# Kernel tuning notes

Hardware: AMD Instinct MI355X
Metric: run time of the kernel (lower is better)

Reference implementation:

```python
import jax, jax.numpy as jnp
import numpy as np

B, NELEC, NATOMS, SH_PER_ATOM, NORB, NCTR = 512, 100, 20, 30, 300, 2
NBAS = NATOMS * SH_PER_ATOM  # 600 == NORB * NCTR


def _ipow(x, k):
    # x**k for integer k in {0,1,2}; safe for negative x (cartesian harmonics)
    return jnp.where(k == 0, jnp.ones_like(x), jnp.where(k == 1, x, x * x))


def setup_inputs() -> dict:
    key = jax.random.key(0)
    ks = jax.random.split(key, 7)
    pos = jax.random.normal(ks[0], (B, NELEC * 3), jnp.float32)
    atom_coords = jax.random.normal(ks[1], (NATOMS, 3), jnp.float32)
    bas_exp = jax.random.uniform(ks[2], (NBAS,), jnp.float32, 0.5, 3.0)
    bas_n = jax.random.randint(ks[3], (NBAS,), 0, 3).astype(jnp.float32)
    norm_cst = jax.random.uniform(ks[4], (NBAS,), jnp.float32, 0.5, 1.5)
    bas_coeffs = jax.random.normal(ks[5], (NBAS,), jnp.float32)
    bas_kxyz = jax.random.randint(ks[6], (NBAS, 3), 0, 3)  # kx, ky, kz exponents
    index_ctr = jnp.repeat(jnp.arange(NORB, dtype=jnp.int32), NCTR)  # nbas -> norb
    return {"pos": pos, "atom_coords": atom_coords, "bas_exp": bas_exp,
            "bas_n": bas_n, "norm_cst": norm_cst, "bas_coeffs": bas_coeffs,
            "bas_kxyz": bas_kxyz, "index_ctr": index_ctr}


def reference(pos, atom_coords, bas_exp, bas_n, norm_cst, bas_coeffs, bas_kxyz, index_ctr):
    # gather: per-shell atom coordinates  (NBAS, 3)
    bas_coords = jnp.repeat(atom_coords, SH_PER_ATOM, axis=0)
    # electron - basis-center displacement  (B, Nelec, NBAS, 3)
    xyz = pos.reshape(-1, NELEC, 1, 3) - bas_coords[None, None]
    r2 = jnp.sum(xyz * xyz, axis=-1)                 # (B, Nelec, NBAS)
    r = jnp.sqrt(r2)
    # radial_gaussian: r^n * exp(-alpha r^2)
    R = jnp.power(r, bas_n) * jnp.exp(-bas_exp * r2)
    # cartesian harmonics: x^kx * y^ky * z^kz
    Y = (_ipow(xyz[..., 0], bas_kxyz[:, 0]) *
         _ipow(xyz[..., 1], bas_kxyz[:, 1]) *
         _ipow(xyz[..., 2], bas_kxyz[:, 2]))
    # ao kernel + contraction (segment-sum over basis fns into orbitals)
    vals = (norm_cst * bas_coeffs) * R * Y           # (B, Nelec, NBAS)
    ao = jnp.zeros((pos.shape[0], NELEC, NORB), vals.dtype).at[:, :, index_ctr].add(vals)
    return ao
```

## Files before the change

### kernel.cpp

```cpp
#include <hip/hip_runtime.h>

#define BATCH   512
#define NELEC   100
#define NATOMS  20
#define SH      30
#define NORB    300
#define NBAS    600
#define NROWS   (BATCH * NELEC)
#define ROWS    16
#define NBLOCKS (NROWS / ROWS)
#define BLOCK   320

#define LOG2E 1.4426950408889634f

__global__ __launch_bounds__(BLOCK, 8) void ao_kernel(
    const float* __restrict__ pos,
    const float* __restrict__ atom_coords,
    const float* __restrict__ bas_exp,
    const float* __restrict__ bas_n,
    const float* __restrict__ norm_cst,
    const float* __restrict__ bas_coeffs,
    const int*   __restrict__ bas_kxyz,
    float*       __restrict__ out)
{
    __shared__ float4 spos4[ROWS];

    const int t    = threadIdx.x;
    const int row0 = blockIdx.x * ROWS;

    if (t < ROWS * 3) {
        ((float*)spos4)[(t / 3) * 4 + (t % 3)] = pos[(size_t)row0 * 3 + t];
    }
    __syncthreads();

    if (t < NORB) {
        const int s0 = 2 * t, s1 = s0 + 1;

        const float c0 = norm_cst[s0] * bas_coeffs[s0];
        const float c1 = norm_cst[s1] * bas_coeffs[s1];
        const float al0 = -bas_exp[s0] * LOG2E;
        const float al1 = -bas_exp[s1] * LOG2E;
        const int n0 = (int)bas_n[s0], n1 = (int)bas_n[s1];
        const float q00 = (n0 == 0) ? c0 : 0.0f, q01 = (n0 == 1) ? c0 : 0.0f, q02 = (n0 == 2) ? c0 : 0.0f;
        const float q10 = (n1 == 0) ? c1 : 0.0f, q11 = (n1 == 1) ? c1 : 0.0f, q12 = (n1 == 2) ? c1 : 0.0f;
        const int kx0 = bas_kxyz[3 * s0 + 0], ky0 = bas_kxyz[3 * s0 + 1], kz0 = bas_kxyz[3 * s0 + 2];
        const int kx1 = bas_kxyz[3 * s1 + 0], ky1 = bas_kxyz[3 * s1 + 1], kz1 = bas_kxyz[3 * s1 + 2];
        const float mx00 = (kx0 == 0), mx01 = (kx0 == 1), mx02 = (kx0 == 2);
        const float my00 = (ky0 == 0), my01 = (ky0 == 1), my02 = (ky0 == 2);
        const float mz00 = (kz0 == 0), mz01 = (kz0 == 1), mz02 = (kz0 == 2);
        const float mx10 = (kx1 == 0), mx11 = (kx1 == 1), mx12 = (kx1 == 2);
        const float my10 = (ky1 == 0), my11 = (ky1 == 1), my12 = (ky1 == 2);
        const float mz10 = (kz1 == 0), mz11 = (kz1 == 1), mz12 = (kz1 == 2);

        const int at = s0 / SH;
        const float ax = atom_coords[3 * at + 0];
        const float ay = atom_coords[3 * at + 1];
        const float az = atom_coords[3 * at + 2];

        float* op = out + (size_t)row0 * NORB + t;

#pragma unroll 4
        for (int r = 0; r < ROWS; ++r) {
            const float4 p = spos4[r];

            const float dx = p.x - ax, dy = p.y - ay, dz = p.z - az;
            const float r2 = fmaf(dx, dx, fmaf(dy, dy, dz * dz));
            const float rr = __builtin_amdgcn_sqrtf(r2);

            float e  = __builtin_amdgcn_exp2f(al0 * r2);
            float cR = fmaf(rr, q01, fmaf(r2, q02, q00));
            float yx = fmaf(dx, fmaf(dx, mx02, mx01), mx00);
            float yy = fmaf(dy, fmaf(dy, my02, my01), my00);
            float yz = fmaf(dz, fmaf(dz, mz02, mz01), mz00);
            float v  = (cR * e) * ((yx * yy) * yz);

            e  = __builtin_amdgcn_exp2f(al1 * r2);
            cR = fmaf(rr, q11, fmaf(r2, q12, q10));
            yx = fmaf(dx, fmaf(dx, mx12, mx11), mx10);
            yy = fmaf(dy, fmaf(dy, my12, my11), my10);
            yz = fmaf(dz, fmaf(dz, mz12, mz11), mz10);
            v  = fmaf(cR * e, (yx * yy) * yz, v);

            *op = v;
            op += NORB;
        }
    }
}

extern "C" void kernel_launch(void* const* d_in, const int* in_sizes, int n_in,
                              void* d_out, int out_size, void* d_ws, size_t ws_size,
                              hipStream_t stream) {
    const float* pos         = (const float*)d_in[0];
    const float* atom_coords = (const float*)d_in[1];
    const float* bas_exp     = (const float*)d_in[2];
    const float* bas_n       = (const float*)d_in[3];
    const float* norm_cst    = (const float*)d_in[4];
    const float* bas_coeffs  = (const float*)d_in[5];
    const int*   bas_kxyz    = (const int*)d_in[6];
    float* out = (float*)d_out;

    ao_kernel<<<NBLOCKS, BLOCK, 0, stream>>>(pos, atom_coords, bas_exp, bas_n,
                                             norm_cst, bas_coeffs, bas_kxyz, out);
}
```

Baseline: 98.66 us.

## Double rows per block, vectorize param loads before barrier, nontemporal stores

Each block now holds two 320-thread groups that each process 16 rows, so a block covers 32 rows and half as many blocks are launched. Per-basis parameters are read as float2/int2 vector loads issued before the barrier, so their latency overlaps the position load. Output writes use nontemporal stores to avoid polluting the cache. The cost is larger blocks, which may reduce scheduling flexibility, and __launch_bounds__(BLOCK, 8) with BLOCK now 640 may constrain register allocation.

```diff
diff --git a/kernel.cpp b/kernel.cpp
--- a/kernel.cpp
+++ b/kernel.cpp
@@ -7,9 +7,11 @@
 #define NORB    300
 #define NBAS    600
 #define NROWS   (BATCH * NELEC)
-#define ROWS    16
+#define GROWS   16
+#define NGRP    2
+#define ROWS    (GROWS * NGRP)
 #define NBLOCKS (NROWS / ROWS)
-#define BLOCK   320
+#define BLOCK   (320 * NGRP)
 
 #define LOG2E 1.4426950408889634f
 
@@ -26,25 +28,43 @@
     __shared__ float4 spos4[ROWS];
 
     const int t    = threadIdx.x;
-    const int row0 = blockIdx.x * ROWS;
+    const int g    = (t >= 320) ? 1 : 0;
+    const int tt   = t - 320 * g;
+    const int brow = blockIdx.x * ROWS;
+    const int row0 = brow + g * GROWS;
+
+    float2 ex2, nn2, nc2, bc2;
+    int2 k01, k23, k45;
+    float ax = 0.f, ay = 0.f, az = 0.f;
+    if (tt < NORB) {
+        ex2 = ((const float2*)bas_exp)[tt];
+        nn2 = ((const float2*)bas_n)[tt];
+        nc2 = ((const float2*)norm_cst)[tt];
+        bc2 = ((const float2*)bas_coeffs)[tt];
+        k01 = ((const int2*)bas_kxyz)[3 * tt + 0];
+        k23 = ((const int2*)bas_kxyz)[3 * tt + 1];
+        k45 = ((const int2*)bas_kxyz)[3 * tt + 2];
+        const int at = (2 * tt) / SH;
+        ax = atom_coords[3 * at + 0];
+        ay = atom_coords[3 * at + 1];
+        az = atom_coords[3 * at + 2];
+    }
 
     if (t < ROWS * 3) {
-        ((float*)spos4)[(t / 3) * 4 + (t % 3)] = pos[(size_t)row0 * 3 + t];
+        ((float*)spos4)[(t / 3) * 4 + (t % 3)] = pos[(size_t)brow * 3 + t];
     }
     __syncthreads();
 
-    if (t < NORB) {
-        const int s0 = 2 * t, s1 = s0 + 1;
-
-        const float c0 = norm_cst[s0] * bas_coeffs[s0];
-        const float c1 = norm_cst[s1] * bas_coeffs[s1];
-        const float al0 = -bas_exp[s0] * LOG2E;
-        const float al1 = -bas_exp[s1] * LOG2E;
-        const int n0 = (int)bas_n[s0], n1 = (int)bas_n[s1];
+    if (tt < NORB) {
+        const float c0 = nc2.x * bc2.x;
+        const float c1 = nc2.y * bc2.y;
+        const float al0 = -ex2.x * LOG2E;
+        const float al1 = -ex2.y * LOG2E;
+        const int n0 = (int)nn2.x, n1 = (int)nn2.y;
         const float q00 = (n0 == 0) ? c0 : 0.0f, q01 = (n0 == 1) ? c0 : 0.0f, q02 = (n0 == 2) ? c0 : 0.0f;
         const float q10 = (n1 == 0) ? c1 : 0.0f, q11 = (n1 == 1) ? c1 : 0.0f, q12 = (n1 == 2) ? c1 : 0.0f;
-        const int kx0 = bas_kxyz[3 * s0 + 0], ky0 = bas_kxyz[3 * s0 + 1], kz0 = bas_kxyz[3 * s0 + 2];
-        const int kx1 = bas_kxyz[3 * s1 + 0], ky1 = bas_kxyz[3 * s1 + 1], kz1 = bas_kxyz[3 * s1 + 2];
+        const int kx0 = k01.x, ky0 = k01.y, kz0 = k23.x;
+        const int kx1 = k23.y, ky1 = k45.x, kz1 = k45.y;
         const float mx00 = (kx0 == 0), mx01 = (kx0 == 1), mx02 = (kx0 == 2);
         const float my00 = (ky0 == 0), my01 = (ky0 == 1), my02 = (ky0 == 2);
         const float mz00 = (kz0 == 0), mz01 = (kz0 == 1), mz02 = (kz0 == 2);
@@ -52,16 +72,11 @@
         const float my10 = (ky1 == 0), my11 = (ky1 == 1), my12 = (ky1 == 2);
         const float mz10 = (kz1 == 0), mz11 = (kz1 == 1), mz12 = (kz1 == 2);
 
-        const int at = s0 / SH;
-        const float ax = atom_coords[3 * at + 0];
-        const float ay = atom_coords[3 * at + 1];
-        const float az = atom_coords[3 * at + 2];
-
-        float* op = out + (size_t)row0 * NORB + t;
+        float* op = out + (size_t)row0 * NORB + tt;
 
 #pragma unroll 4
-        for (int r = 0; r < ROWS; ++r) {
-            const float4 p = spos4[r];
+        for (int r = 0; r < GROWS; ++r) {
+            const float4 p = spos4[g * GROWS + r];
 
             const float dx = p.x - ax, dy = p.y - ay, dz = p.z - az;
             const float r2 = fmaf(dx, dx, fmaf(dy, dy, dz * dz));
@@ -81,7 +96,7 @@
             yz = fmaf(dz, fmaf(dz, mz12, mz11), mz10);
             v  = fmaf(cR * e, (yx * yy) * yz, v);
 
-            *op = v;
+            __builtin_nontemporal_store(v, op);
             op += NORB;
         }
     }
```

Result: slower. 102.4 us (+3.8%).
